# Performance work log

Measured on AMD Instinct MI355X. Metric: run time of the kernel, lower is better.

Reference implementation:

```python
import jax, jax.numpy as jnp
import numpy as np

# FitzHugh-Nagumo / Model_FN constants (from __init__)
A_ = 0.7; B_ = 0.8; EPI = 0.2; TAU = 0.1; I_ = 1.0; K_ = 1.0; W_ = 1.0
STRENGTH = 1.0; UMAX = 10.0; D_SM = 0.1; EPS_REG = 1e-3
DIM = 1024; N = 4096


def smooth_relu(x, d=D_SM):
    r = jnp.maximum(x, 0.0)
    sq = (2.0 * d * r ** 3 - r ** 4) / (2.0 * d ** 3)
    return jnp.where(r < d, sq, x - d / 2.0)


def temp_L(t, P):
    # vectorized version of Model_FN.temp_L: sum_i eig_i * v_i^T v_i, i=1..dim-1
    dim = P.shape[0]
    i = jnp.arange(1, dim)
    s = 2.0 * K_ * jnp.sin(W_ * t)                      # [1]
    thresh = int(dim + 1) / 2 - 1                       # float threshold, as in source
    eig = jnp.where(i <= thresh, 1.0 + s, 1.0 - s)      # [dim-1]
    V = P[1:]                                           # [dim-1, dim]
    return V.T @ (eig[:, None] * V)                     # [dim, dim]


def control_net(x, W1, b1, W2, b2, W3, b3):
    # ControlNet.forward: u = MLP(x); bound(u * x)
    h1 = jnp.tanh(x @ W1.T + b1)
    h2 = jnp.tanh(h1 @ W2.T + b2)
    u = h2 @ W3.T + b3
    ux = u * x
    ux = jnp.where(ux < UMAX, ux, 0.0)
    return jnp.where(-UMAX < ux, ux, 0.0)


def icnn_fn(x, ws, bs, us):
    # ICNN.icnn_fn: x [N, d_in] -> z [1, N]
    xt = x.T                                            # [d_in, N]
    z = smooth_relu(ws[0] @ xt + bs[0])
    for i in range(len(us)):
        z = smooth_relu(ws[i + 1] @ xt + bs[i + 1] + jax.nn.softplus(us[i]) @ z)
    return z


def setup_inputs() -> dict:
    key = jax.random.key(0)
    ks = jax.random.split(key, 20)
    d_in = 2 * DIM
    inp = {
        'state': jax.random.normal(ks[0], (N, d_in), jnp.float32),
        't': jax.random.uniform(ks[1], (1,), jnp.float32) * 10.0,
        'P': jax.random.normal(ks[2], (DIM, DIM), jnp.float32) / np.sqrt(DIM),
        # ControlNet weights (SpectralNorm wrapper undefined in source -> plain Linear)
        'W1': jax.random.normal(ks[3], (512, d_in), jnp.float32) / np.sqrt(d_in),
        'b1': jax.random.normal(ks[4], (512,), jnp.float32) * 0.01,
        'W2': jax.random.normal(ks[5], (512, 512), jnp.float32) / np.sqrt(512),
        'b2': jax.random.normal(ks[6], (512,), jnp.float32) * 0.01,
        'W3': jax.random.normal(ks[7], (d_in, 512), jnp.float32) / np.sqrt(512),
        'b3': jax.random.normal(ks[8], (d_in,), jnp.float32) * 0.01,
        # ICNN parameters, layer_sizes=[64, 64, 1]
        'icW0': jax.random.normal(ks[9], (64, d_in), jnp.float32) / np.sqrt(d_in),
        'icb0': jax.random.normal(ks[10], (64, 1), jnp.float32) * 0.01,
        'icW1': jax.random.normal(ks[11], (64, d_in), jnp.float32) / np.sqrt(d_in),
        'icb1': jax.random.normal(ks[12], (64, 1), jnp.float32) * 0.01,
        'icW2': jax.random.normal(ks[13], (1, d_in), jnp.float32) / np.sqrt(d_in),
        'icb2': jax.random.normal(ks[14], (1, 1), jnp.float32) * 0.01,
        'icU0': jax.random.normal(ks[15], (64, 64), jnp.float32) / np.sqrt(64),
        'icU1': jax.random.normal(ks[16], (1, 64), jnp.float32) / np.sqrt(64),
    }
    return inp


def reference(state, t, P, W1, b1, W2, b2, W3, b3,
              icW0, icb0, icW1, icb1, icW2, icb2, icU0, icU1):
    dim = state.shape[1] // 2
    u, v = state[:, :dim], state[:, dim:]

    # FN drift with time-varying Laplacian coupling (Model_FN.FN)
    Lm = temp_L(t, P)                                   # [dim, dim]
    Hu = jax.nn.sigmoid(u / TAU)                        # H(u)
    du = u - u ** 3 / 3.0 - v + I_ + STRENGTH * (Hu @ Lm.T)
    dv = EPI * (u + A_ - B_ * v)
    dx = jnp.concatenate([du, dv], axis=1)              # [N, 2*dim]

    # ControlNet on synchronization deviations (Model_FN.FN_g state transform)
    st = jnp.concatenate([u - u[:, :1], v - v[:, :1]], axis=1)
    ctrl = control_net(st, W1, b1, W2, b2, W3, b3)
    dx_total = dx + ctrl

    # ICNN Lyapunov value (ICNN.forward)
    ws, bs, us = [icW0, icW1, icW2], [icb0, icb1, icb2], [icU0, icU1]
    z = icnn_fn(state, ws, bs, us)                      # [1, N]
    z0 = icnn_fn(jnp.zeros_like(state), ws, bs, us)     # [1, N]
    regular = EPS_REG * jnp.sum(state ** 2, axis=1, keepdims=True)
    V = smooth_relu(z - z0).T + regular                 # [N, 1]

    return jnp.concatenate([dx_total, V], axis=1)       # [N, 2*dim + 1]
```

## Files before the change

kernel.cpp:

```cpp
#include <hip/hip_runtime.h>
#include <hip/hip_fp8.h>
#include <cstdint>
#include <cstddef>

using short8 = __attribute__((ext_vector_type(8))) short;
using f32x4  = __attribute__((ext_vector_type(4))) float;
using bfraw  = unsigned short;

__device__ __forceinline__ bfraw f2b(float f){
  unsigned int u = __builtin_bit_cast(unsigned int, f);
  u += 0x7FFFu + ((u >> 16) & 1u);
  return (bfraw)(u >> 16);
}
__device__ __forceinline__ float b2f(bfraw h){
  unsigned int u = ((unsigned int)h) << 16;
  return __builtin_bit_cast(float, u);
}
__device__ __forceinline__ unsigned char f2f8(float f){
  __hip_fp8_e4m3 t(f);
  return (unsigned char)t.__x;
}
__device__ __forceinline__ float srelu(float x){
  float r = fmaxf(x, 0.0f);
  if (r < 0.1f){ float r2 = r * r; return (0.2f * r2 * r - r2 * r2) * 500.0f; }
  return x - 0.05f;
}
__device__ __forceinline__ float softplusf(float x){
  return (x > 15.0f) ? x : log1pf(expf(x));
}
__device__ __forceinline__ void gload16(const void* g, void* s){
  __builtin_amdgcn_global_load_lds((const __attribute__((address_space(1))) void*)g,
                                   (__attribute__((address_space(3))) void*)s, 16, 0, 0);
}
template<int N> __device__ __forceinline__ void wait_vm(){
  if constexpr (N == 0)      asm volatile("s_waitcnt vmcnt(0)" ::: "memory");
  else if constexpr (N == 2) asm volatile("s_waitcnt vmcnt(2)" ::: "memory");
  else if constexpr (N == 3) asm volatile("s_waitcnt vmcnt(3)" ::: "memory");
  else                       asm volatile("s_waitcnt vmcnt(4)" ::: "memory");
}
__device__ __forceinline__ void block_barrier(){
  __builtin_amdgcn_s_barrier();
  asm volatile("" ::: "memory");
}

constexpr size_t OFF_STATEB = 0;
constexpr size_t OFF_HUB    = 16777216;
constexpr size_t OFF_PT     = 20971520;
constexpr size_t OFF_PTEIG  = 23068672;
constexpr size_t OFF_LM8    = 25165824;
constexpr size_t OFF_W1ZB   = 26214400;
constexpr size_t OFF_W2B    = 28835840;
constexpr size_t OFF_W38    = 29360128;
constexpr size_t OFF_H1B    = 30408704;
constexpr size_t OFF_H28    = 34603008;
constexpr size_t OFF_Z1F    = 36700160;
constexpr size_t OFF_Z2PRE  = 37748736;
constexpr size_t OFF_SPU0   = 38797312;
constexpr size_t OFF_SPU1   = 38813696;
constexpr size_t OFF_Z0     = 38813952;
constexpr size_t OFF_SU1    = 38814208;
constexpr size_t OFF_SV1    = 38816256;
constexpr size_t OFF_U0     = 38818304;
constexpr size_t OFF_V0     = 38834688;

__global__ __launch_bounds__(256) void prep_all(const float* __restrict__ W1,
    const float* __restrict__ icW0, const float* __restrict__ icW1,
    const float* __restrict__ W2, const float* __restrict__ W3,
    const float* __restrict__ P, const float* __restrict__ tptr,
    const float* __restrict__ icU0, const float* __restrict__ icU1,
    const float* __restrict__ icb0, const float* __restrict__ icb1, const float* __restrict__ icb2,
    const float* __restrict__ state,
    bfraw* __restrict__ w1zb, bfraw* __restrict__ w2b, unsigned char* __restrict__ w3f8,
    bfraw* __restrict__ PT, bfraw* __restrict__ PTeig,
    float* __restrict__ su1, float* __restrict__ sv1,
    float* __restrict__ spU0, float* __restrict__ spU1, float* __restrict__ z0out,
    bfraw* __restrict__ stateb, unsigned char* __restrict__ hub8,
    float* __restrict__ u0a, float* __restrict__ v0a){
  __shared__ float smem[4288];
  const int b = blockIdx.x;
  const int t = threadIdx.x;
  if (b < 2560){
    const int i4 = (b * 256 + t) * 4;
    if (i4 < 1572864){
      const float* src; bfraw* dst; int off;
      if (i4 < 1048576)      { src = W1;   dst = w1zb;           off = i4; }
      else if (i4 < 1179648) { src = icW0; dst = w1zb + 1048576; off = i4 - 1048576; }
      else if (i4 < 1310720) { src = icW1; dst = w1zb + 1179648; off = i4 - 1179648; }
      else                   { src = W2;   dst = w2b;            off = i4 - 1310720; }
      float4 v = *reinterpret_cast<const float4*>(src + off);
      ushort4 o;
      o.x = f2b(v.x); o.y = f2b(v.y); o.z = f2b(v.z); o.w = f2b(v.w);
      *reinterpret_cast<ushort4*>(dst + off) = o;
    } else {
      const int off = i4 - 1572864;
      float4 v = *reinterpret_cast<const float4*>(W3 + off);
      uchar4 o;
      o.x = f2f8(v.x); o.y = f2f8(v.y); o.z = f2f8(v.z); o.w = f2f8(v.w);
      *reinterpret_cast<uchar4*>(w3f8 + off) = o;
    }
  } else if (b < 3584){
    float (*tile)[33] = (float(*)[33])smem;
    const int idx = b - 2560;
    const int bi = idx >> 5, bj = idx & 31;
    const int tx = t & 31, ty = t >> 5;
    #pragma unroll
    for (int r = 0; r < 4; ++r){
      const int k = bj * 32 + ty + r * 8;
      const int i = bi * 32 + tx;
      tile[ty + r * 8][tx] = P[(size_t)k * 1024 + i];
    }
    __syncthreads();
    const float s = 2.0f * sinf(tptr[0]);
    #pragma unroll
    for (int r = 0; r < 4; ++r){
      const int i = bi * 32 + ty + r * 8;
      const int k = bj * 32 + tx;
      const float p = tile[tx][ty + r * 8];
      const float e = (k == 0) ? 0.0f : ((k <= 511) ? (1.0f + s) : (1.0f - s));
      PT[(size_t)i * 1024 + k] = f2b(p);
      PTeig[(size_t)i * 1024 + k] = f2b(e * p);
    }
  } else if (b < 4096){
    const int n = b - 3584;
    float a = 0.0f, bb = 0.0f;
    for (int j = t; j < 1024; j += 256) a += W1[(size_t)n * 2048 + j];
    for (int j = t; j < 1024; j += 256) bb += W1[(size_t)n * 2048 + 1024 + j];
    #pragma unroll
    for (int o = 32; o > 0; o >>= 1){ a += __shfl_down(a, o, 64); bb += __shfl_down(bb, o, 64); }
    if ((t & 63) == 0){ smem[t >> 6] = a; smem[4 + (t >> 6)] = bb; }
    __syncthreads();
    if (t == 0){
      su1[n] = smem[0] + smem[1] + smem[2] + smem[3];
      sv1[n] = smem[4] + smem[5] + smem[6] + smem[7];
    }
  } else if (b == 4096){
    float* sp  = smem;
    float* sp1 = smem + 4096;
    float* a0  = smem + 4160;
    float* a1  = smem + 4224;
    #pragma unroll
    for (int i = 0; i < 16; ++i){
      const int idx = i * 256 + t;
      const float v = softplusf(icU0[idx]);
      sp[idx] = v;
      spU0[idx] = v;
    }
    if (t < 64){
      const float v1 = softplusf(icU1[t]);
      sp1[t] = v1;
      spU1[t] = v1;
      a0[t] = srelu(icb0[t]);
    }
    __syncthreads();
    {
      const int n = t >> 2, q = t & 3;
      float sAcc = 0.0f;
      #pragma unroll
      for (int j = 0; j < 16; ++j) sAcc += sp[n * 64 + q * 16 + j] * a0[q * 16 + j];
      sAcc += __shfl_down(sAcc, 2, 64);
      sAcc += __shfl_down(sAcc, 1, 64);
      if (q == 0) a1[n] = srelu(sAcc + icb1[n]);
    }
    __syncthreads();
    if (t < 64){
      float v = sp1[t] * a1[t];
      #pragma unroll
      for (int o = 32; o > 0; o >>= 1) v += __shfl_down(v, o, 64);
      if (t == 0) z0out[0] = srelu(v + icb2[0]);
    }
  } else {
    const int row = b - 4097;
    const float* srow = state + (size_t)row * 2048;
    float4 u4 = *reinterpret_cast<const float4*>(srow + t * 4);
    float4 v4 = *reinterpret_cast<const float4*>(srow + 1024 + t * 4);
    float us[4] = {u4.x, u4.y, u4.z, u4.w};
    float vs[4] = {v4.x, v4.y, v4.z, v4.w};
    uchar4 h8;
    unsigned char* hp = reinterpret_cast<unsigned char*>(&h8);
    #pragma unroll
    for (int i = 0; i < 4; ++i){
      const int j = t * 4 + i;
      const float u = us[i], v = vs[i];
      stateb[(size_t)row * 2048 + j] = f2b(u);
      stateb[(size_t)row * 2048 + 1024 + j] = f2b(v);
      hp[i] = f2f8(1.0f / (1.0f + expf(-10.0f * u)));
    }
    *reinterpret_cast<uchar4*>(hub8 + (size_t)row * 1024 + t * 4) = h8;
    if (t == 0){ u0a[row] = srow[0]; v0a[row] = srow[1024]; }
  }
}

__global__ __launch_bounds__(256) void v2_kernel(const bfraw* __restrict__ stateb, const float* __restrict__ icW2,
    const float* __restrict__ z1f, const float* __restrict__ z2pre,
    const float* __restrict__ spU0, const float* __restrict__ spU1,
    const float* __restrict__ z0p, const float* __restrict__ icb2, float* __restrict__ out){
  const int row = blockIdx.x;
  const int t = threadIdx.x;
  __shared__ float z1s[64];
  __shared__ float s1[4], s2[4];
  if (t < 64) z1s[t] = z1f[(size_t)row * 64 + t];
  short8 xv = reinterpret_cast<const short8*>(stateb + (size_t)row * 2048)[t];
  float4 w0 = reinterpret_cast<const float4*>(icW2)[t * 2];
  float4 w1 = reinterpret_cast<const float4*>(icW2)[t * 2 + 1];
  float wv[8] = {w0.x, w0.y, w0.z, w0.w, w1.x, w1.y, w1.z, w1.w};
  float d = 0.0f, ss = 0.0f;
  #pragma unroll
  for (int e = 0; e < 8; ++e){
    const float x = b2f((bfraw)xv[e]);
    d  = fmaf(wv[e], x, d);
    ss = fmaf(x, x, ss);
  }
  #pragma unroll
  for (int o = 32; o > 0; o >>= 1){ d += __shfl_down(d, o, 64); ss += __shfl_down(ss, o, 64); }
  if ((t & 63) == 0){ s1[t >> 6] = d; s2[t >> 6] = ss; }
  __syncthreads();
  if (t < 64){
    float acc2 = z2pre[(size_t)row * 64 + t];
    #pragma unroll 8
    for (int j = 0; j < 64; ++j) acc2 += spU0[t * 64 + j] * z1s[j];
    float dd = spU1[t] * srelu(acc2);
    #pragma unroll
    for (int o = 32; o > 0; o >>= 1) dd += __shfl_down(dd, o, 64);
    if (t == 0){
      const float D = dd + s1[0] + s1[1] + s1[2] + s1[3];
      const float S = s2[0] + s2[1] + s2[2] + s2[3];
      const float z3 = srelu(D + icb2[0]);
      out[(size_t)row * 2049 + 2048] = srelu(z3 - z0p[0]) + 0.001f * S;
    }
  }
}

template<int EPI, int TM, int TN>
__global__ __launch_bounds__(512)
void gemm_nt(const bfraw* __restrict__ A, const bfraw* __restrict__ B,
             int N, int K,
             const float* __restrict__ bias,
             bfraw* __restrict__ outb, unsigned char* __restrict__ outf8,
             const float* __restrict__ u0a, const float* __restrict__ v0a,
             const float* __restrict__ su1, const float* __restrict__ sv1,
             const float* __restrict__ icb0, const float* __restrict__ icb1,
             float* __restrict__ z1f, float* __restrict__ z2pre)
{
  constexpr int MF = TM / 32;
  constexpr int NF = TN / 64;
  constexpr int LPB = TM / 64 + TN / 64;
  __shared__ bfraw lA[3][TM * 64];
  __shared__ bfraw lB[3][TN * 64];
  const int tid = threadIdx.x;
  const int w  = tid >> 6;
  const int l  = tid & 63;
  const int wr = w >> 2;
  const int wc = w & 3;
  const int bm = blockIdx.x;
  const int bn = blockIdx.y;
  const int lr = l & 15;
  const int q  = l >> 4;

  f32x4 acc[MF][NF] = {};
  const int nt = K >> 6;

  auto stage = [&](int buf, int k0){
    #pragma unroll
    for (int j = 0; j < TM / 64; ++j){
      const int c = j * 512 + tid;
      const int r = c >> 3;
      const int kc = (c & 7) ^ (r & 7);
      gload16(A + (size_t)(bm * TM + r) * K + k0 + kc * 8, &lA[buf][(size_t)(j * 512 + w * 64) * 8]);
    }
    #pragma unroll
    for (int j = 0; j < TN / 64; ++j){
      const int c = j * 512 + tid;
      const int r = c >> 3;
      const int kc = (c & 7) ^ (r & 7);
      gload16(B + (size_t)(bn * TN + r) * K + k0 + kc * 8, &lB[buf][(size_t)(j * 512 + w * 64) * 8]);
    }
  };

  stage(0, 0);
  stage(1, 64);
  for (int t = 0; t < nt; ++t){
    const int cur = t % 3;
    if (t == nt - 1) wait_vm<0>(); else wait_vm<LPB>();
    block_barrier();
    short8 aF[2][MF], bF[2][NF];
    #pragma unroll
    for (int kh = 0; kh < 2; ++kh){
      #pragma unroll
      for (int m = 0; m < MF; ++m){
        const int R = wr * (TM / 2) + m * 16 + lr;
        const int kch = (kh * 4 + q) ^ (lr & 7);
        aF[kh][m] = *reinterpret_cast<const short8*>(&lA[cur][(size_t)R * 64 + kch * 8]);
      }
      #pragma unroll
      for (int n = 0; n < NF; ++n){
        const int R = wc * (TN / 4) + n * 16 + lr;
        const int kch = (kh * 4 + q) ^ (lr & 7);
        bF[kh][n] = *reinterpret_cast<const short8*>(&lB[cur][(size_t)R * 64 + kch * 8]);
      }
    }
    if (t + 2 < nt) stage((t + 2) % 3, (t + 2) * 64);
    #pragma unroll
    for (int kh = 0; kh < 2; ++kh){
      #pragma unroll
      for (int m = 0; m < MF; ++m){
        #pragma unroll
        for (int n = 0; n < NF; ++n){
          acc[m][n] = __builtin_amdgcn_mfma_f32_16x16x32_bf16(aF[kh][m], bF[kh][n], acc[m][n], 0, 0, 0);
        }
      }
    }
  }

  #pragma unroll
  for (int m = 0; m < MF; ++m){
    #pragma unroll
    for (int n = 0; n < NF; ++n){
      #pragma unroll
      for (int r = 0; r < 4; ++r){
        const int row = bm * TM + wr * (TM / 2) + m * 16 + q * 4 + r;
        const int col = bn * TN + wc * (TN / 4) + n * 16 + lr;
        const float v = acc[m][n][r];
        if constexpr (EPI == 0){
          outf8[(size_t)row * N + col] = f2f8(v);
        } else if constexpr (EPI == 2){
          outf8[(size_t)row * N + col] = f2f8(tanhf(v + bias[col]));
        } else if constexpr (EPI == 4){
          if (col < 512){
            const float h = v - u0a[row] * su1[col] - v0a[row] * sv1[col] + bias[col];
            outb[(size_t)row * 512 + col] = f2b(tanhf(h));
          } else if (col < 576){
            z1f[(size_t)row * 64 + (col - 512)] = srelu(v + icb0[col - 512]);
          } else {
            z2pre[(size_t)row * 64 + (col - 576)] = v + icb1[col - 576];
          }
        }
      }
    }
  }
}

__global__ __launch_bounds__(512, 4)
void gemm_out(const unsigned char* __restrict__ hub8, const unsigned char* __restrict__ lm8,
              const unsigned char* __restrict__ h2b8, const unsigned char* __restrict__ w3f8,
              const bfraw* __restrict__ stateb, const float* __restrict__ b3,
              const float* __restrict__ u0a, const float* __restrict__ v0a,
              float* __restrict__ out)
{
  __shared__ unsigned char lA[128 * 128];
  __shared__ unsigned char lBlo[64 * 128];
  __shared__ unsigned char lBhi[64 * 128];
  const int tid = threadIdx.x;
  const int w  = tid >> 6;
  const int l  = tid & 63;
  const int wr = w >> 2;
  const int wc = w & 3;
  const int bm = blockIdx.x;
  const int bn = blockIdx.y;
  const int lr = l & 15;
  const int q  = l >> 4;

  const unsigned char* Au  = h2b8 + (size_t)(bm * 128) * 512;
  const unsigned char* Bwl = w3f8 + (size_t)(bn * 64) * 512;
  const unsigned char* Bwh = w3f8 + (size_t)(1024 + bn * 64) * 512;
  const unsigned char* Ah  = hub8 + (size_t)(bm * 128) * 1024;
  const unsigned char* Bl  = lm8  + (size_t)(bn * 64) * 1024;

  f32x4 acc2[4] = {};
  f32x4 acc3[4] = {};

  for (int t = 0; t < 4; ++t){
    const int k0 = t * 128;
    #pragma unroll
    for (int j = 0; j < 2; ++j){
      const int c = j * 512 + tid;
      const int r = c >> 3;
      const int kc = (c & 7) ^ (r & 7);
      gload16(Au + (size_t)r * 512 + k0 + kc * 16, &lA[(size_t)(j * 512 + w * 64) * 16]);
    }
    {
      const int r = tid >> 3;
      const int kc = (tid & 7) ^ (r & 7);
      gload16(Bwl + (size_t)r * 512 + k0 + kc * 16, &lBlo[(size_t)(w * 64) * 16]);
      gload16(Bwh + (size_t)r * 512 + k0 + kc * 16, &lBhi[(size_t)(w * 64) * 16]);
    }
    __syncthreads();
    #pragma unroll
    for (int kh = 0; kh < 4; ++kh){
      const int ko = kh * 32 + q * 8;
      const int ch = (ko >> 4) ^ (lr & 7);
      const int bo = ko & 15;
      long long aF[4], bL, bH;
      #pragma unroll
      for (int m = 0; m < 4; ++m){
        const int R = wr * 64 + m * 16 + lr;
        aF[m] = *reinterpret_cast<const long long*>(&lA[(size_t)R * 128 + ch * 16 + bo]);
      }
      const int Rb = wc * 16 + lr;
      bL = *reinterpret_cast<const long long*>(&lBlo[(size_t)Rb * 128 + ch * 16 + bo]);
      bH = *reinterpret_cast<const long long*>(&lBhi[(size_t)Rb * 128 + ch * 16 + bo]);
      #pragma unroll
      for (int m = 0; m < 4; ++m){
        acc2[m] = __builtin_amdgcn_mfma_f32_16x16x32_fp8_fp8(aF[m], bL, acc2[m], 0, 0, 0);
        acc3[m] = __builtin_amdgcn_mfma_f32_16x16x32_fp8_fp8(aF[m], bH, acc3[m], 0, 0, 0);
      }
    }
    __syncthreads();
  }

  #pragma unroll
  for (int m = 0; m < 4; ++m){
    #pragma unroll
    for (int r = 0; r < 4; ++r){
      const int row = bm * 128 + wr * 64 + m * 16 + q * 4 + r;
      const int c   = bn * 64 + wc * 16 + lr;
      const float un = acc3[m][r] + b3[1024 + c];
      const float u  = b2f(stateb[(size_t)row * 2048 + c]);
      const float vv = b2f(stateb[(size_t)row * 2048 + 1024 + c]);
      const float x  = vv - v0a[row];
      const float ux = un * x;
      const float cl = (ux < 10.0f && -10.0f < ux) ? ux : 0.0f;
      out[(size_t)row * 2049 + 1024 + c] = 0.2f * (u + 0.7f - 0.8f * vv) + cl;
    }
  }

  f32x4 acc1[4] = {};
  for (int t = 0; t < 8; ++t){
    const int k0 = t * 128;
    #pragma unroll
    for (int j = 0; j < 2; ++j){
      const int c = j * 512 + tid;
      const int r = c >> 3;
      const int kc = (c & 7) ^ (r & 7);
      gload16(Ah + (size_t)r * 1024 + k0 + kc * 16, &lA[(size_t)(j * 512 + w * 64) * 16]);
    }
    {
      const int r = tid >> 3;
      const int kc = (tid & 7) ^ (r & 7);
      gload16(Bl + (size_t)r * 1024 + k0 + kc * 16, &lBlo[(size_t)(w * 64) * 16]);
    }
    __syncthreads();
    #pragma unroll
    for (int kh = 0; kh < 4; ++kh){
      const int ko = kh * 32 + q * 8;
      const int ch = (ko >> 4) ^ (lr & 7);
      const int bo = ko & 15;
      long long aF[4], bL;
      #pragma unroll
      for (int m = 0; m < 4; ++m){
        const int R = wr * 64 + m * 16 + lr;
        aF[m] = *reinterpret_cast<const long long*>(&lA[(size_t)R * 128 + ch * 16 + bo]);
      }
      const int Rb = wc * 16 + lr;
      bL = *reinterpret_cast<const long long*>(&lBlo[(size_t)Rb * 128 + ch * 16 + bo]);
      #pragma unroll
      for (int m = 0; m < 4; ++m){
        acc1[m] = __builtin_amdgcn_mfma_f32_16x16x32_fp8_fp8(aF[m], bL, acc1[m], 0, 0, 0);
      }
    }
    __syncthreads();
  }

  #pragma unroll
  for (int m = 0; m < 4; ++m){
    #pragma unroll
    for (int r = 0; r < 4; ++r){
      const int row = bm * 128 + wr * 64 + m * 16 + q * 4 + r;
      const int c   = bn * 64 + wc * 16 + lr;
      const float un = acc2[m][r] + b3[c];
      const float u  = b2f(stateb[(size_t)row * 2048 + c]);
      const float vv = b2f(stateb[(size_t)row * 2048 + 1024 + c]);
      const float x  = u - u0a[row];
      const float ux = un * x;
      const float cl = (ux < 10.0f && -10.0f < ux) ? ux : 0.0f;
      out[(size_t)row * 2049 + c] = acc1[m][r] + u - u * u * u * (1.0f / 3.0f) - vv + 1.0f + cl;
    }
  }
}

extern "C" void kernel_launch(void* const* d_in, const int* in_sizes, int n_in,
                              void* d_out, int out_size, void* d_ws, size_t ws_size,
                              hipStream_t stream){
  (void)in_sizes; (void)n_in; (void)out_size; (void)ws_size;
  const float* state = (const float*)d_in[0];
  const float* tp    = (const float*)d_in[1];
  const float* P     = (const float*)d_in[2];
  const float* W1    = (const float*)d_in[3];
  const float* b1    = (const float*)d_in[4];
  const float* W2    = (const float*)d_in[5];
  const float* b2    = (const float*)d_in[6];
  const float* W3    = (const float*)d_in[7];
  const float* b3    = (const float*)d_in[8];
  const float* icW0  = (const float*)d_in[9];
  const float* icb0  = (const float*)d_in[10];
  const float* icW1  = (const float*)d_in[11];
  const float* icb1  = (const float*)d_in[12];
  const float* icW2  = (const float*)d_in[13];
  const float* icb2  = (const float*)d_in[14];
  const float* icU0  = (const float*)d_in[15];
  const float* icU1  = (const float*)d_in[16];
  float* out = (float*)d_out;
  char* ws = (char*)d_ws;

  bfraw* stateb = (bfraw*)(ws + OFF_STATEB);
  unsigned char* hub8 = (unsigned char*)(ws + OFF_HUB);
  bfraw* pt     = (bfraw*)(ws + OFF_PT);
  bfraw* pteig  = (bfraw*)(ws + OFF_PTEIG);
  unsigned char* lm8  = (unsigned char*)(ws + OFF_LM8);
  bfraw* w1zb   = (bfraw*)(ws + OFF_W1ZB);
  bfraw* w2b    = (bfraw*)(ws + OFF_W2B);
  unsigned char* w3f8 = (unsigned char*)(ws + OFF_W38);
  bfraw* h1b    = (bfraw*)(ws + OFF_H1B);
  unsigned char* h28  = (unsigned char*)(ws + OFF_H28);
  float* z1f    = (float*)(ws + OFF_Z1F);
  float* z2pre  = (float*)(ws + OFF_Z2PRE);
  float* spU0   = (float*)(ws + OFF_SPU0);
  float* spU1   = (float*)(ws + OFF_SPU1);
  float* z0     = (float*)(ws + OFF_Z0);
  float* su1    = (float*)(ws + OFF_SU1);
  float* sv1    = (float*)(ws + OFF_SV1);
  float* u0a    = (float*)(ws + OFF_U0);
  float* v0a    = (float*)(ws + OFF_V0);

  prep_all<<<dim3(8193), 256, 0, stream>>>(W1, icW0, icW1, W2, W3, P, tp,
      icU0, icU1, icb0, icb1, icb2, state,
      w1zb, w2b, w3f8, pt, pteig, su1, sv1, spU0, spU1, z0,
      stateb, hub8, u0a, v0a);

  gemm_nt<0, 64, 64><<<dim3(16, 16), 512, 0, stream>>>(pteig, pt, 1024, 1024,
      nullptr, nullptr, lm8, nullptr, nullptr, nullptr, nullptr, nullptr, nullptr, nullptr, nullptr);
  gemm_nt<4, 64, 128><<<dim3(64, 5), 512, 0, stream>>>(stateb, w1zb, 640, 2048,
      b1, h1b, nullptr, u0a, v0a, su1, sv1, icb0, icb1, z1f, z2pre);
  gemm_nt<2, 64, 128><<<dim3(64, 4), 512, 0, stream>>>(h1b, w2b, 512, 512,
      b2, nullptr, h28, nullptr, nullptr, nullptr, nullptr, nullptr, nullptr, nullptr, nullptr);
  gemm_out<<<dim3(32, 16), 512, 0, stream>>>(hub8, lm8, h28, w3f8, stateb, b3, u0a, v0a, out);

  v2_kernel<<<dim3(4096), 256, 0, stream>>>(stateb, icW2, z1f, z2pre, spU0, spU1, z0, icb2, out);
}
```

Before: 100.7 us.

## Move ControlNet layer GEMMs to FP8 MFMA and merge Laplacian with ICNN GEMM

The ControlNet first and second layer GEMMs now use FP8 operands (state, W1, h1, W2) with the fp8 16x16x32 MFMA and a 128-wide K tile, in place of bf16. This halves operand bytes and raises MFMA throughput. The Laplacian P^T·diag·P GEMM and the ICNN first-layer GEMM are merged into one new bf16 kernel launch, so ICNN stays in bf16. The cost is an extra fp8 copy of the state written in prep, and lower precision in the control-net path.

```diff
diff --git a/kernel.cpp b/kernel.cpp
--- a/kernel.cpp
+++ b/kernel.cpp
@@ -44,24 +44,26 @@
 }
 
 constexpr size_t OFF_STATEB = 0;
-constexpr size_t OFF_HUB    = 16777216;
-constexpr size_t OFF_PT     = 20971520;
-constexpr size_t OFF_PTEIG  = 23068672;
-constexpr size_t OFF_LM8    = 25165824;
-constexpr size_t OFF_W1ZB   = 26214400;
-constexpr size_t OFF_W2B    = 28835840;
-constexpr size_t OFF_W38    = 29360128;
-constexpr size_t OFF_H1B    = 30408704;
-constexpr size_t OFF_H28    = 34603008;
-constexpr size_t OFF_Z1F    = 36700160;
-constexpr size_t OFF_Z2PRE  = 37748736;
-constexpr size_t OFF_SPU0   = 38797312;
-constexpr size_t OFF_SPU1   = 38813696;
-constexpr size_t OFF_Z0     = 38813952;
-constexpr size_t OFF_SU1    = 38814208;
-constexpr size_t OFF_SV1    = 38816256;
-constexpr size_t OFF_U0     = 38818304;
-constexpr size_t OFF_V0     = 38834688;
+constexpr size_t OFF_STATE8 = 16777216;
+constexpr size_t OFF_HUB    = 25165824;
+constexpr size_t OFF_PT     = 29360128;
+constexpr size_t OFF_PTEIG  = 31457280;
+constexpr size_t OFF_LM8    = 33554432;
+constexpr size_t OFF_W1F8   = 34603008;
+constexpr size_t OFF_ICWB   = 35651584;
+constexpr size_t OFF_W28    = 36175872;
+constexpr size_t OFF_W38    = 36438016;
+constexpr size_t OFF_H18    = 37486592;
+constexpr size_t OFF_H28    = 39583744;
+constexpr size_t OFF_Z1F    = 41680896;
+constexpr size_t OFF_Z2PRE  = 42729472;
+constexpr size_t OFF_SPU0   = 43778048;
+constexpr size_t OFF_SPU1   = 43794432;
+constexpr size_t OFF_Z0     = 43794688;
+constexpr size_t OFF_SU1    = 43794944;
+constexpr size_t OFF_SV1    = 43796992;
+constexpr size_t OFF_U0     = 43799040;
+constexpr size_t OFF_V0     = 43815424;
 
 __global__ __launch_bounds__(256) void prep_all(const float* __restrict__ W1,
     const float* __restrict__ icW0, const float* __restrict__ icW1,
@@ -70,33 +72,35 @@
     const float* __restrict__ icU0, const float* __restrict__ icU1,
     const float* __restrict__ icb0, const float* __restrict__ icb1, const float* __restrict__ icb2,
     const float* __restrict__ state,
-    bfraw* __restrict__ w1zb, bfraw* __restrict__ w2b, unsigned char* __restrict__ w3f8,
+    unsigned char* __restrict__ w1f8, bfraw* __restrict__ icwb,
+    unsigned char* __restrict__ w28, unsigned char* __restrict__ w3f8,
     bfraw* __restrict__ PT, bfraw* __restrict__ PTeig,
     float* __restrict__ su1, float* __restrict__ sv1,
     float* __restrict__ spU0, float* __restrict__ spU1, float* __restrict__ z0out,
-    bfraw* __restrict__ stateb, unsigned char* __restrict__ hub8,
+    bfraw* __restrict__ stateb, unsigned char* __restrict__ state8, unsigned char* __restrict__ hub8,
     float* __restrict__ u0a, float* __restrict__ v0a){
   __shared__ float smem[4288];
   const int b = blockIdx.x;
   const int t = threadIdx.x;
   if (b < 2560){
     const int i4 = (b * 256 + t) * 4;
-    if (i4 < 1572864){
-      const float* src; bfraw* dst; int off;
-      if (i4 < 1048576)      { src = W1;   dst = w1zb;           off = i4; }
-      else if (i4 < 1179648) { src = icW0; dst = w1zb + 1048576; off = i4 - 1048576; }
-      else if (i4 < 1310720) { src = icW1; dst = w1zb + 1179648; off = i4 - 1179648; }
-      else                   { src = W2;   dst = w2b;            off = i4 - 1310720; }
+    if (i4 >= 1048576 && i4 < 1310720){
+      const float* src = (i4 < 1179648) ? icW0 : icW1;
+      const int off = (i4 < 1179648) ? (i4 - 1048576) : (i4 - 1179648);
+      const int dsto = i4 - 1048576;
       float4 v = *reinterpret_cast<const float4*>(src + off);
       ushort4 o;
       o.x = f2b(v.x); o.y = f2b(v.y); o.z = f2b(v.z); o.w = f2b(v.w);
-      *reinterpret_cast<ushort4*>(dst + off) = o;
+      *reinterpret_cast<ushort4*>(icwb + dsto) = o;
     } else {
-      const int off = i4 - 1572864;
-      float4 v = *reinterpret_cast<const float4*>(W3 + off);
+      const float* src; unsigned char* dst; int off;
+      if (i4 < 1048576)      { src = W1; dst = w1f8; off = i4; }
+      else if (i4 < 1572864) { src = W2; dst = w28;  off = i4 - 1310720; }
+      else                   { src = W3; dst = w3f8; off = i4 - 1572864; }
+      float4 v = *reinterpret_cast<const float4*>(src + off);
       uchar4 o;
       o.x = f2f8(v.x); o.y = f2f8(v.y); o.z = f2f8(v.z); o.w = f2f8(v.w);
-      *reinterpret_cast<uchar4*>(w3f8 + off) = o;
+      *reinterpret_cast<uchar4*>(dst + off) = o;
     }
   } else if (b < 3584){
     float (*tile)[33] = (float(*)[33])smem;
@@ -175,16 +179,22 @@
     float4 v4 = *reinterpret_cast<const float4*>(srow + 1024 + t * 4);
     float us[4] = {u4.x, u4.y, u4.z, u4.w};
     float vs[4] = {v4.x, v4.y, v4.z, v4.w};
-    uchar4 h8;
+    uchar4 h8, s8u, s8v;
     unsigned char* hp = reinterpret_cast<unsigned char*>(&h8);
+    unsigned char* su = reinterpret_cast<unsigned char*>(&s8u);
+    unsigned char* sv = reinterpret_cast<unsigned char*>(&s8v);
     #pragma unroll
     for (int i = 0; i < 4; ++i){
       const int j = t * 4 + i;
       const float u = us[i], v = vs[i];
       stateb[(size_t)row * 2048 + j] = f2b(u);
       stateb[(size_t)row * 2048 + 1024 + j] = f2b(v);
+      su[i] = f2f8(u);
+      sv[i] = f2f8(v);
       hp[i] = f2f8(1.0f / (1.0f + expf(-10.0f * u)));
     }
+    *reinterpret_cast<uchar4*>(state8 + (size_t)row * 2048 + t * 4) = s8u;
+    *reinterpret_cast<uchar4*>(state8 + (size_t)row * 2048 + 1024 + t * 4) = s8v;
     *reinterpret_cast<uchar4*>(hub8 + (size_t)row * 1024 + t * 4) = h8;
     if (t == 0){ u0a[row] = srow[0]; v0a[row] = srow[1024]; }
   }
@@ -230,22 +240,95 @@
   }
 }
 
+__global__ __launch_bounds__(512)
+void gemm_mid(const bfraw* __restrict__ pteig, const bfraw* __restrict__ pt,
+              unsigned char* __restrict__ lm8,
+              const bfraw* __restrict__ stateb, const bfraw* __restrict__ icwb,
+              const float* __restrict__ icb0, const float* __restrict__ icb1,
+              float* __restrict__ z1f, float* __restrict__ z2pre)
+{
+  __shared__ bfraw lA[3][64 * 64];
+  __shared__ bfraw lB[3][64 * 64];
+  const int blk = blockIdx.x;
+  const bool isLm = (blk < 256);
+  const bfraw* A; const bfraw* B; int K, bm, bn;
+  if (isLm){ A = pteig; B = pt; K = 1024; bm = blk >> 4; bn = blk & 15; }
+  else     { const int i = blk - 256; A = stateb; B = icwb; K = 2048; bm = i >> 1; bn = i & 1; }
+  const int tid = threadIdx.x;
+  const int w  = tid >> 6;
+  const int l  = tid & 63;
+  const int wr = w >> 2;
+  const int wc = w & 3;
+  const int lr = l & 15;
+  const int q  = l >> 4;
+
+  f32x4 acc[2] = {};
+  const int nt = K >> 6;
+
+  auto stage = [&](int buf, int k0){
+    const int r = tid >> 3;
+    const int kc = (tid & 7) ^ (r & 7);
+    gload16(A + (size_t)(bm * 64 + r) * K + k0 + kc * 8, &lA[buf][(size_t)(w * 64) * 8]);
+    gload16(B + (size_t)(bn * 64 + r) * K + k0 + kc * 8, &lB[buf][(size_t)(w * 64) * 8]);
+  };
+
+  stage(0, 0);
+  stage(1, 64);
+  for (int t = 0; t < nt; ++t){
+    const int cur = t % 3;
+    if (t == nt - 1) wait_vm<0>(); else wait_vm<2>();
+    block_barrier();
+    short8 aF[2][2], bF[2];
+    #pragma unroll
+    for (int kh = 0; kh < 2; ++kh){
+      const int kch = (kh * 4 + q) ^ (lr & 7);
+      #pragma unroll
+      for (int m = 0; m < 2; ++m){
+        const int R = wr * 32 + m * 16 + lr;
+        aF[kh][m] = *reinterpret_cast<const short8*>(&lA[cur][(size_t)R * 64 + kch * 8]);
+      }
+      const int R = wc * 16 + lr;
+      bF[kh] = *reinterpret_cast<const short8*>(&lB[cur][(size_t)R * 64 + kch * 8]);
+    }
+    if (t + 2 < nt) stage((t + 2) % 3, (t + 2) * 64);
+    #pragma unroll
+    for (int kh = 0; kh < 2; ++kh)
+      #pragma unroll
+      for (int m = 0; m < 2; ++m)
+        acc[m] = __builtin_amdgcn_mfma_f32_16x16x32_bf16(aF[kh][m], bF[kh], acc[m], 0, 0, 0);
+  }
+
+  #pragma unroll
+  for (int m = 0; m < 2; ++m){
+    #pragma unroll
+    for (int r = 0; r < 4; ++r){
+      const int row = bm * 64 + wr * 32 + m * 16 + q * 4 + r;
+      const int c64 = wc * 16 + lr;
+      const float v = acc[m][r];
+      if (isLm){
+        lm8[(size_t)row * 1024 + bn * 64 + c64] = f2f8(v);
+      } else if (bn == 0){
+        z1f[(size_t)row * 64 + c64] = srelu(v + icb0[c64]);
+      } else {
+        z2pre[(size_t)row * 64 + c64] = v + icb1[c64];
+      }
+    }
+  }
+}
+
 template<int EPI, int TM, int TN>
 __global__ __launch_bounds__(512)
-void gemm_nt(const bfraw* __restrict__ A, const bfraw* __restrict__ B,
-             int N, int K,
-             const float* __restrict__ bias,
-             bfraw* __restrict__ outb, unsigned char* __restrict__ outf8,
-             const float* __restrict__ u0a, const float* __restrict__ v0a,
-             const float* __restrict__ su1, const float* __restrict__ sv1,
-             const float* __restrict__ icb0, const float* __restrict__ icb1,
-             float* __restrict__ z1f, float* __restrict__ z2pre)
+void gemm_nt8(const unsigned char* __restrict__ A, const unsigned char* __restrict__ B,
+              int N, int K,
+              const float* __restrict__ bias, unsigned char* __restrict__ outf8,
+              const float* __restrict__ u0a, const float* __restrict__ v0a,
+              const float* __restrict__ su1, const float* __restrict__ sv1)
 {
   constexpr int MF = TM / 32;
   constexpr int NF = TN / 64;
   constexpr int LPB = TM / 64 + TN / 64;
-  __shared__ bfraw lA[3][TM * 64];
-  __shared__ bfraw lB[3][TN * 64];
+  __shared__ unsigned char lA[3][TM * 128];
+  __shared__ unsigned char lB[3][TN * 128];
   const int tid = threadIdx.x;
   const int w  = tid >> 6;
   const int l  = tid & 63;
@@ -257,7 +340,7 @@
   const int q  = l >> 4;
 
   f32x4 acc[MF][NF] = {};
-  const int nt = K >> 6;
+  const int nt = K >> 7;
 
   auto stage = [&](int buf, int k0){
     #pragma unroll
@@ -265,47 +348,48 @@
       const int c = j * 512 + tid;
       const int r = c >> 3;
       const int kc = (c & 7) ^ (r & 7);
-      gload16(A + (size_t)(bm * TM + r) * K + k0 + kc * 8, &lA[buf][(size_t)(j * 512 + w * 64) * 8]);
+      gload16(A + (size_t)(bm * TM + r) * K + k0 + kc * 16, &lA[buf][(size_t)(j * 512 + w * 64) * 16]);
     }
     #pragma unroll
     for (int j = 0; j < TN / 64; ++j){
       const int c = j * 512 + tid;
       const int r = c >> 3;
       const int kc = (c & 7) ^ (r & 7);
-      gload16(B + (size_t)(bn * TN + r) * K + k0 + kc * 8, &lB[buf][(size_t)(j * 512 + w * 64) * 8]);
+      gload16(B + (size_t)(bn * TN + r) * K + k0 + kc * 16, &lB[buf][(size_t)(j * 512 + w * 64) * 16]);
     }
   };
 
   stage(0, 0);
-  stage(1, 64);
+  stage(1, 128);
   for (int t = 0; t < nt; ++t){
     const int cur = t % 3;
     if (t == nt - 1) wait_vm<0>(); else wait_vm<LPB>();
     block_barrier();
-    short8 aF[2][MF], bF[2][NF];
-    #pragma unroll
-    for (int kh = 0; kh < 2; ++kh){
+    long long aF[4][MF], bF[4][NF];
+    #pragma unroll
+    for (int kh = 0; kh < 4; ++kh){
+      const int ko = kh * 32 + q * 8;
+      const int ch = (ko >> 4) ^ (lr & 7);
+      const int bo = ko & 15;
       #pragma unroll
       for (int m = 0; m < MF; ++m){
         const int R = wr * (TM / 2) + m * 16 + lr;
-        const int kch = (kh * 4 + q) ^ (lr & 7);
-        aF[kh][m] = *reinterpret_cast<const short8*>(&lA[cur][(size_t)R * 64 + kch * 8]);
+        aF[kh][m] = *reinterpret_cast<const long long*>(&lA[cur][(size_t)R * 128 + ch * 16 + bo]);
       }
       #pragma unroll
       for (int n = 0; n < NF; ++n){
         const int R = wc * (TN / 4) + n * 16 + lr;
-        const int kch = (kh * 4 + q) ^ (lr & 7);
-        bF[kh][n] = *reinterpret_cast<const short8*>(&lB[cur][(size_t)R * 64 + kch * 8]);
-      }
-    }
-    if (t + 2 < nt) stage((t + 2) % 3, (t + 2) * 64);
-    #pragma unroll
-    for (int kh = 0; kh < 2; ++kh){
+        bF[kh][n] = *reinterpret_cast<const long long*>(&lB[cur][(size_t)R * 128 + ch * 16 + bo]);
+      }
+    }
+    if (t + 2 < nt) stage((t + 2) % 3, (t + 2) * 128);
+    #pragma unroll
+    for (int kh = 0; kh < 4; ++kh){
       #pragma unroll
       for (int m = 0; m < MF; ++m){
         #pragma unroll
         for (int n = 0; n < NF; ++n){
-          acc[m][n] = __builtin_amdgcn_mfma_f32_16x16x32_bf16(aF[kh][m], bF[kh][n], acc[m][n], 0, 0, 0);
+          acc[m][n] = __builtin_amdgcn_mfma_f32_16x16x32_fp8_fp8(aF[kh][m], bF[kh][n], acc[m][n], 0, 0, 0);
         }
       }
     }
@@ -320,19 +404,11 @@
         const int row = bm * TM + wr * (TM / 2) + m * 16 + q * 4 + r;
         const int col = bn * TN + wc * (TN / 4) + n * 16 + lr;
         const float v = acc[m][n][r];
-        if constexpr (EPI == 0){
-          outf8[(size_t)row * N + col] = f2f8(v);
-        } else if constexpr (EPI == 2){
+        if constexpr (EPI == 1){
+          const float h = v - u0a[row] * su1[col] - v0a[row] * sv1[col] + bias[col];
+          outf8[(size_t)row * N + col] = f2f8(tanhf(h));
+        } else {
           outf8[(size_t)row * N + col] = f2f8(tanhf(v + bias[col]));
-        } else if constexpr (EPI == 4){
-          if (col < 512){
-            const float h = v - u0a[row] * su1[col] - v0a[row] * sv1[col] + bias[col];
-            outb[(size_t)row * 512 + col] = f2b(tanhf(h));
-          } else if (col < 576){
-            z1f[(size_t)row * 64 + (col - 512)] = srelu(v + icb0[col - 512]);
-          } else {
-            z2pre[(size_t)row * 64 + (col - 576)] = v + icb1[col - 576];
-          }
         }
       }
     }
@@ -502,14 +578,16 @@
   char* ws = (char*)d_ws;
 
   bfraw* stateb = (bfraw*)(ws + OFF_STATEB);
-  unsigned char* hub8 = (unsigned char*)(ws + OFF_HUB);
+  unsigned char* state8 = (unsigned char*)(ws + OFF_STATE8);
+  unsigned char* hub8   = (unsigned char*)(ws + OFF_HUB);
   bfraw* pt     = (bfraw*)(ws + OFF_PT);
   bfraw* pteig  = (bfraw*)(ws + OFF_PTEIG);
   unsigned char* lm8  = (unsigned char*)(ws + OFF_LM8);
-  bfraw* w1zb   = (bfraw*)(ws + OFF_W1ZB);
-  bfraw* w2b    = (bfraw*)(ws + OFF_W2B);
+  unsigned char* w1f8 = (unsigned char*)(ws + OFF_W1F8);
+  bfraw* icwb   = (bfraw*)(ws + OFF_ICWB);
+  unsigned char* w28  = (unsigned char*)(ws + OFF_W28);
   unsigned char* w3f8 = (unsigned char*)(ws + OFF_W38);
-  bfraw* h1b    = (bfraw*)(ws + OFF_H1B);
+  unsigned char* h18  = (unsigned char*)(ws + OFF_H18);
   unsigned char* h28  = (unsigned char*)(ws + OFF_H28);
   float* z1f    = (float*)(ws + OFF_Z1F);
   float* z2pre  = (float*)(ws + OFF_Z2PRE);
@@ -523,15 +601,14 @@
 
   prep_all<<<dim3(8193), 256, 0, stream>>>(W1, icW0, icW1, W2, W3, P, tp,
       icU0, icU1, icb0, icb1, icb2, state,
-      w1zb, w2b, w3f8, pt, pteig, su1, sv1, spU0, spU1, z0,
-      stateb, hub8, u0a, v0a);
-
-  gemm_nt<0, 64, 64><<<dim3(16, 16), 512, 0, stream>>>(pteig, pt, 1024, 1024,
-      nullptr, nullptr, lm8, nullptr, nullptr, nullptr, nullptr, nullptr, nullptr, nullptr, nullptr);
-  gemm_nt<4, 64, 128><<<dim3(64, 5), 512, 0, stream>>>(stateb, w1zb, 640, 2048,
-      b1, h1b, nullptr, u0a, v0a, su1, sv1, icb0, icb1, z1f, z2pre);
-  gemm_nt<2, 64, 128><<<dim3(64, 4), 512, 0, stream>>>(h1b, w2b, 512, 512,
-      b2, nullptr, h28, nullptr, nullptr, nullptr, nullptr, nullptr, nullptr, nullptr, nullptr);
+      w1f8, icwb, w28, w3f8, pt, pteig, su1, sv1, spU0, spU1, z0,
+      stateb, state8, hub8, u0a, v0a);
+
+  gemm_mid<<<dim3(384), 512, 0, stream>>>(pteig, pt, lm8, stateb, icwb, icb0, icb1, z1f, z2pre);
+  gemm_nt8<1, 64, 128><<<dim3(64, 4), 512, 0, stream>>>(state8, w1f8, 512, 2048,
+      b1, h18, u0a, v0a, su1, sv1);
+  gemm_nt8<2, 64, 128><<<dim3(64, 4), 512, 0, stream>>>(h18, w28, 512, 512,
+      b2, h28, nullptr, nullptr, nullptr, nullptr);
   gemm_out<<<dim3(32, 16), 512, 0, stream>>>(hub8, lm8, h28, w3f8, stateb, b3, u0a, v0a, out);
 
   v2_kernel<<<dim3(4096), 256, 0, stream>>>(stateb, icW2, z1f, z2pre, spU0, spU1, z0, icb2, out);
```

Measured after the change: 101.5 us. Within noise of the previous version (+0.8%).
